# Optimization experiments

Measured on AMD Instinct MI355X. Metric: run time of the kernel, lower is better.

The kernel has to match this reference:

```python
import jax, jax.numpy as jnp
import numpy as np

H = 2048      # hidden_size
K = 16        # n_memory_tokens
NQ = K + 2    # extraction queries (+halt, +value)
NH = 4        # extraction heads
HD = H // NH  # head dim = 512
FFN = 2 * H   # ffn_mult=2
MAXE = 128    # memory buffer capacity (full -> eviction path)
B, S = 4, 4096
EPS = 1e-6


def setup_inputs() -> dict:
    key = jax.random.key(0)
    ks = jax.random.split(key, 20)
    r = lambda i, shape, s=0.02: jax.random.normal(ks[i], shape, jnp.float32) * s
    return {
        "hidden_states": jax.random.normal(ks[0], (B, S, H), jnp.float32),
        "buf_entries": jax.random.normal(ks[1], (MAXE, H), jnp.float32),
        "buf_priorities": jax.random.uniform(ks[2], (MAXE,), jnp.float32),
        "queries": r(3, (NQ, H)),
        "Wq": r(4, (H, H)), "Wk": r(5, (H, H)), "Wv": r(6, (H, H)), "Wo": r(7, (H, H)),
        "ln_w": jnp.ones((H,), jnp.float32),
        "Wgate": r(8, (FFN, H)), "Wup": r(9, (FFN, H)), "Wdown": r(10, (H, FFN)),
        "Wp": r(11, (1, H)), "bp": jnp.full((1,), 0.5, jnp.float32),
        "Wh": r(12, (1, H)), "bh": jnp.full((1,), 1.0, jnp.float32),
        "V1": r(13, (H, 2 * H)), "b1": jnp.zeros((H,), jnp.float32),
        "V2": r(14, (H // 4, H)), "b2": jnp.zeros((H // 4,), jnp.float32),
        "V3": jnp.zeros((1, H // 4), jnp.float32), "b3": jnp.zeros((1,), jnp.float32),
    }


def reference(hidden_states, buf_entries, buf_priorities, queries,
              Wq, Wk, Wv, Wo, ln_w, Wgate, Wup, Wdown,
              Wp, bp, Wh, bh, V1, b1, V2, b2, V3, b3):
    b = hidden_states.shape[0]
    # --- cross-attention: NQ learned queries attend over hidden states ---
    q = (queries @ Wq.T).reshape(NQ, NH, HD)               # queries shared across batch
    k = (hidden_states @ Wk.T).reshape(b, -1, NH, HD)      # (b, s, h, d)
    v = (hidden_states @ Wv.T).reshape(b, -1, NH, HD)
    scores = jnp.einsum('qhd,bshd->bhqs', q, k) / jnp.sqrt(jnp.float32(HD))
    attn = jax.nn.softmax(scores, axis=-1)
    out = jnp.einsum('bhqs,bshd->bqhd', attn, v).reshape(b, NQ, H)
    extracted = out @ Wo.T
    memory_raw = extracted[:, :K]            # (b, K, H)
    confidence_vec = extracted[:, K]         # (b, H)
    value_vec = extracted[:, K + 1]          # (b, H)
    # --- RMSNorm + SwiGLU FFN residual (dropout = identity in eval) ---
    ms = jnp.mean(memory_raw * memory_raw, axis=-1, keepdims=True)
    xn = memory_raw * jax.lax.rsqrt(ms + EPS) * ln_w
    ffn = (jax.nn.silu(xn @ Wgate.T) * (xn @ Wup.T)) @ Wdown.T
    memory = memory_raw + ffn
    # --- heads ---
    priority = jax.nn.sigmoid(memory @ Wp.T + bp)[..., 0]          # (b, K)
    confidence = jax.nn.sigmoid(confidence_vec @ Wh.T + bh)[..., 0]  # (b,)
    value_input = jnp.concatenate([value_vec, hidden_states[:, -1, :]], axis=-1)
    h1 = jax.nn.silu(value_input @ V1.T + b1)
    h2 = jax.nn.silu(h1 @ V2.T + b2)
    value = (h2 @ V3.T + b3)[..., 0]                               # (b,)
    # --- MemoryBuffer.store with full buffer: sequential priority eviction ---
    # (torch loops K times with argmin().item() host syncs; lax.scan preserves
    #  the sequential compare-and-replace semantics in one fused program)
    vecs = jax.lax.stop_gradient(memory[0])     # store detaches; uses batch 0
    pris = jax.lax.stop_gradient(priority[0])

    def step(carry, xp):
        ent, pr = carry
        vec, p = xp
        idx = jnp.argmin(pr)
        take = p > pr[idx]
        ent = ent.at[idx].set(jnp.where(take, vec, ent[idx]))
        pr = pr.at[idx].set(jnp.where(take, p, pr[idx]))
        return (ent, pr), None

    (new_entries, new_priorities), _ = jax.lax.scan(step, (buf_entries, buf_priorities), (vecs, pris))
    return memory, priority, confidence, value, new_entries, new_priorities
```

## Files before the change

kernel.cpp:

```cpp
#include <hip/hip_runtime.h>

#define SS    4096
#define HH    2048
#define NQQ   18
#define QH    72
#define SCALE_F 0.044194173824159216f

#define OUT_MEM     0
#define OUT_PRI     131072
#define OUT_CONF    131136
#define OUT_VAL     131140
#define OUT_ENT     131144
#define OUT_NEWPRI  393288

typedef float  f32x4  __attribute__((ext_vector_type(4)));
typedef __bf16 bf16x8 __attribute__((ext_vector_type(8)));

#define DEVFN static __device__ __forceinline__

DEVFN bf16x8 pack8(f32x4 lo, f32x4 hi){
  bf16x8 r;
  #pragma unroll
  for (int i = 0; i < 4; i++){ r[i] = (__bf16)lo[i]; r[i+4] = (__bf16)hi[i]; }
  return r;
}
DEVFN float siluf(float x){ return x / (1.f + expf(-x)); }
DEVFN float block_sum(float v, float* sb){
  #pragma unroll
  for (int o = 32; o > 0; o >>= 1) v += __shfl_xor(v, o);
  int wid = threadIdx.x >> 6, lane = threadIdx.x & 63;
  if (lane == 0) sb[wid] = v;
  __syncthreads();
  v = sb[0] + sb[1] + sb[2] + sb[3];
  __syncthreads();
  return v;
}

template<int MF, int KC, bool HSEL>
__global__ __launch_bounds__(256) void gemm_bt(
    const __bf16* __restrict__ A, int Kf,
    const float* __restrict__ B0, float* __restrict__ C0,
    const float* __restrict__ B1, float* __restrict__ C1,
    int N)
{
  constexpr int Mp = 16 * MF;
  const int lane = threadIdx.x & 63, w = threadIdx.x >> 6;
  const int n0 = blockIdx.x * 64 + w * 16;
  const int k0 = blockIdx.y * KC * 32;
  const float* B = blockIdx.z ? B1 : B0;
  float* Cp      = blockIdx.z ? C1 : C0;
  const __bf16* aBase = A + (HSEL ? (long)(n0 >> 9) * Mp * Kf : 0)
                          + (long)(lane & 15) * Kf + k0 + 8 * (lane >> 4);
  const float* bBase = B + (long)(n0 + (lane & 15)) * Kf + k0 + 8 * (lane >> 4);
  f32x4 acc[MF];
  #pragma unroll
  for (int m = 0; m < MF; m++) acc[m] = (f32x4)(0.f);
  #pragma unroll 4
  for (int c = 0; c < KC; c++){
    f32x4 lo = *reinterpret_cast<const f32x4*>(bBase + c * 32);
    f32x4 hi = *reinterpret_cast<const f32x4*>(bBase + c * 32 + 4);
    bf16x8 bb = pack8(lo, hi);
    #pragma unroll
    for (int m = 0; m < MF; m++){
      bf16x8 aa = *reinterpret_cast<const bf16x8*>(aBase + (long)m * 16 * Kf + c * 32);
      acc[m] = __builtin_amdgcn_mfma_f32_16x16x32_bf16(aa, bb, acc[m], 0, 0, 0);
    }
  }
  float* cp = Cp + (long)blockIdx.y * Mp * N;
  int row0 = 4 * (lane >> 4), col = n0 + (lane & 15);
  #pragma unroll
  for (int m = 0; m < MF; m++)
    #pragma unroll
    for (int r = 0; r < 4; r++)
      cp[(long)(m * 16 + row0 + r) * N + col] = acc[m][r];
}

template<int MF, int KC>
__global__ __launch_bounds__(256) void gemm_abnat(
    const __bf16* __restrict__ A, long aBatch, int aStride,
    const float* __restrict__ Bn, long bBatch,
    float* __restrict__ Cp, long cBatch,
    int N)
{
  constexpr int Mp = 16 * MF;
  const int lane = threadIdx.x & 63, w = threadIdx.x >> 6;
  const int z = blockIdx.z;
  const int n0 = blockIdx.x * 64 + w * 16;
  const int k0 = blockIdx.y * KC * 32;
  const __bf16* aBase = A + z * aBatch + (long)(lane & 15) * aStride + k0 + 8 * (lane >> 4);
  const float* bBase = Bn + z * bBatch + (long)(k0 + 8 * (lane >> 4)) * N + n0 + (lane & 15);
  f32x4 acc[MF];
  #pragma unroll
  for (int m = 0; m < MF; m++) acc[m] = (f32x4)(0.f);
  #pragma unroll 2
  for (int c = 0; c < KC; c++){
    const float* bp = bBase + (long)c * 32 * N;
    bf16x8 bb;
    #pragma unroll
    for (int j = 0; j < 8; j++) bb[j] = (__bf16)bp[(long)j * N];
    #pragma unroll
    for (int m = 0; m < MF; m++){
      bf16x8 aa = *reinterpret_cast<const bf16x8*>(aBase + (long)m * 16 * aStride + c * 32);
      acc[m] = __builtin_amdgcn_mfma_f32_16x16x32_bf16(aa, bb, acc[m], 0, 0, 0);
    }
  }
  float* cp = Cp + z * cBatch + (long)blockIdx.y * Mp * N;
  int row0 = 4 * (lane >> 4), col = n0 + (lane & 15);
  #pragma unroll
  for (int m = 0; m < MF; m++)
    #pragma unroll
    for (int r = 0; r < 4; r++)
      cp[(long)(m * 16 + row0 + r) * N + col] = acc[m][r];
}

template<int KC>
__global__ __launch_bounds__(256) void gemm_pass1(
    const float* __restrict__ hs, const __bf16* __restrict__ qk,
    float* __restrict__ Sp)
{
  const int lane = threadIdx.x & 63, w = threadIdx.x >> 6;
  const int b = blockIdx.z;
  const int s0 = blockIdx.x * 64 + w * 16;
  const int k0 = blockIdx.y * KC * 32;
  const float* aBase = hs + ((long)b * SS + s0 + (lane & 15)) * HH + k0 + 8 * (lane >> 4);
  const __bf16* bBase = qk + (long)(lane & 15) * HH + k0 + 8 * (lane >> 4);
  f32x4 acc[5];
  #pragma unroll
  for (int n = 0; n < 5; n++) acc[n] = (f32x4)(0.f);
  #pragma unroll 4
  for (int c = 0; c < KC; c++){
    f32x4 lo = *reinterpret_cast<const f32x4*>(aBase + c * 32);
    f32x4 hi = *reinterpret_cast<const f32x4*>(aBase + c * 32 + 4);
    bf16x8 aa = pack8(lo, hi);
    #pragma unroll
    for (int n = 0; n < 5; n++){
      bf16x8 bb = *reinterpret_cast<const bf16x8*>(bBase + (long)n * 16 * HH + c * 32);
      acc[n] = __builtin_amdgcn_mfma_f32_16x16x32_bf16(aa, bb, acc[n], 0, 0, 0);
    }
  }
  float* sp = Sp + ((long)blockIdx.y * 4 + b) * 80 * SS;
  int scol = s0 + 4 * (lane >> 4);
  #pragma unroll
  for (int n = 0; n < 5; n++){
    int qh = n * 16 + (lane & 15);
    *reinterpret_cast<f32x4*>(sp + (long)qh * SS + scol) = acc[n];
  }
}

__global__ void k_prep_qA(const float* __restrict__ queries, __bf16* __restrict__ qA){
  int i = blockIdx.x * 256 + threadIdx.x;
  int r = i >> 11;
  qA[i] = (__bf16)((r < NQQ) ? queries[i] : 0.f);
}
__global__ void k_mkQ2(const float* __restrict__ q_p, __bf16* __restrict__ Q2){
  int i = blockIdx.x * 256 + threadIdx.x;
  int qh = i >> 11, e = i & 2047;
  float v = 0.f;
  if (qh < QH){
    int h = qh / NQQ, qq = qh - h * NQQ;
    if ((e >> 9) == h){
      float s = 0.f;
      #pragma unroll
      for (int y = 0; y < 16; y++) s += q_p[(long)y * 32 * 2048 + qq * 2048 + e];
      v = s * SCALE_F;
    }
  }
  Q2[i] = (__bf16)v;
}
__global__ void k_mkqk(const float* __restrict__ qk_p, __bf16* __restrict__ qk_bf){
  int i = blockIdx.x * 256 + threadIdx.x;
  float s = 0.f;
  #pragma unroll
  for (int y = 0; y < 16; y++) s += qk_p[(long)y * 80 * 2048 + i];
  qk_bf[i] = (__bf16)s;
}
__global__ __launch_bounds__(256) void k_softmax(const float* __restrict__ Sp, __bf16* __restrict__ attn){
  int qh = blockIdx.x, b = blockIdx.y;
  __bf16* arow = attn + ((long)b * 80 + qh) * SS;
  if (qh >= QH){
    #pragma unroll
    for (int it = 0; it < 16; it++) arow[threadIdx.x + 256 * it] = (__bf16)0.f;
    return;
  }
  const float* r0 = Sp + ((long)b * 80 + qh) * SS;
  const long ys = (long)4 * 80 * SS;
  float x[16]; float mx = -1e30f;
  #pragma unroll
  for (int it = 0; it < 16; it++){
    int s = threadIdx.x + 256 * it;
    x[it] = (r0[s] + r0[s + ys]) + (r0[s + 2 * ys] + r0[s + 3 * ys]);
    mx = fmaxf(mx, x[it]);
  }
  __shared__ float sb[8];
  #pragma unroll
  for (int o = 32; o > 0; o >>= 1) mx = fmaxf(mx, __shfl_xor(mx, o));
  int wid = threadIdx.x >> 6, lane = threadIdx.x & 63;
  if (lane == 0) sb[wid] = mx;
  __syncthreads();
  mx = fmaxf(fmaxf(sb[0], sb[1]), fmaxf(sb[2], sb[3]));
  float sum = 0.f;
  #pragma unroll
  for (int it = 0; it < 16; it++){ x[it] = expf(x[it] - mx); sum += x[it]; }
  #pragma unroll
  for (int o = 32; o > 0; o >>= 1) sum += __shfl_xor(sum, o);
  if (lane == 0) sb[4 + wid] = sum;
  __syncthreads();
  sum = sb[4] + sb[5] + sb[6] + sb[7];
  float inv = 1.f / sum;
  #pragma unroll
  for (int it = 0; it < 16; it++) arow[threadIdx.x + 256 * it] = (__bf16)(x[it] * inv);
}
__global__ void k_pack_wv(const float* __restrict__ w_p, __bf16* __restrict__ Apack){
  int i = blockIdx.x * 256 + threadIdx.x;
  int h = i / (80 * 2048);
  int r = (i / 2048) % 80;
  int e = i & 2047;
  float v = 0.f;
  if (r < QH){
    int b = r / NQQ, qq = r - b * NQQ;
    const float* base = w_p + ((long)b * 8 * 80 + (h * NQQ + qq)) * 2048 + e;
    #pragma unroll
    for (int y = 0; y < 8; y++) v += base[(long)y * 80 * 2048];
  }
  Apack[i] = (__bf16)v;
}
__global__ void k_sum_outB(const float* __restrict__ outB_p, __bf16* __restrict__ outB){
  int i = blockIdx.x * 256 + threadIdx.x;
  float s = 0.f;
  #pragma unroll
  for (int y = 0; y < 16; y++) s += outB_p[(long)y * 80 * 2048 + i];
  outB[i] = (__bf16)s;
}
__global__ __launch_bounds__(256) void k_rms(const float* __restrict__ ext_p, const float* __restrict__ ln_w,
                                             const float* __restrict__ hs,
                                             float* __restrict__ extracted, __bf16* __restrict__ xnb,
                                             __bf16* __restrict__ vi){
  int r = blockIdx.x;
  if (r >= 80){
    if (r < 84){
      int b = r - 80;
      const float* src = hs + ((long)b * SS + (SS - 1)) * HH;
      #pragma unroll
      for (int it = 0; it < 8; it++){
        int e = threadIdx.x + 256 * it;
        vi[(long)b * 4096 + 2048 + e] = (__bf16)src[e];
      }
    } else {
      int row = 4 + (r - 84);
      #pragma unroll
      for (int it = 0; it < 16; it++)
        vi[(long)row * 4096 + threadIdx.x + 256 * it] = (__bf16)0.f;
    }
    return;
  }
  float xv[8]; float ss = 0.f;
  #pragma unroll
  for (int it = 0; it < 8; it++){
    int e = threadIdx.x + 256 * it;
    float s = 0.f;
    #pragma unroll
    for (int y = 0; y < 16; y++) s += ext_p[((long)y * 80 + r) * 2048 + e];
    extracted[(long)r * 2048 + e] = s;
    xv[it] = s;
    ss += s * s;
  }
  if (r >= QH) return;
  int b = r / NQQ, qq = r - b * NQQ;
  if (qq < 16){
    __shared__ float sb[4];
    ss = block_sum(ss, sb);
    float inv = 1.f / sqrtf(ss * (1.f / 2048.f) + 1e-6f);
    __bf16* dst = xnb + (long)(b * 16 + qq) * HH;
    #pragma unroll
    for (int it = 0; it < 8; it++){
      int e = threadIdx.x + 256 * it;
      dst[e] = (__bf16)(xv[it] * inv * ln_w[e]);
    }
  } else if (qq == 17){
    #pragma unroll
    for (int it = 0; it < 8; it++){
      int e = threadIdx.x + 256 * it;
      vi[(long)b * 4096 + e] = (__bf16)xv[it];
    }
  }
}
__global__ void k_act(const float* __restrict__ gate_p, const float* __restrict__ up_p,
                      __bf16* __restrict__ hb){
  int i = blockIdx.x * 256 + threadIdx.x;
  float g = 0.f, u = 0.f;
  #pragma unroll
  for (int y = 0; y < 4; y++){
    g += gate_p[(long)y * 64 * 4096 + i];
    u += up_p[(long)y * 64 * 4096 + i];
  }
  hb[i] = (__bf16)(siluf(g) * u);
}
__global__ void k_h1act(const float* __restrict__ h1_p, const float* __restrict__ b1,
                        __bf16* __restrict__ h1s){
  int i = blockIdx.x * 256 + threadIdx.x;
  int r = i >> 11, e = i & 2047;
  float v = 0.f;
  if (r < 4){
    float s = 0.f;
    #pragma unroll
    for (int y = 0; y < 16; y++) s += h1_p[(long)y * 16 * 2048 + i];
    v = siluf(s + b1[e]);
  }
  h1s[i] = (__bf16)v;
}
__global__ __launch_bounds__(256) void k_epilogue(
    const float* __restrict__ extracted, const float* __restrict__ ffn_p,
    const float* __restrict__ h2_p,
    const float* __restrict__ Wp, const float* __restrict__ bp,
    const float* __restrict__ Wh, const float* __restrict__ bh,
    const float* __restrict__ b2, const float* __restrict__ V3, const float* __restrict__ b3,
    float* __restrict__ out)
{
  __shared__ float sb[4];
  int blk = blockIdx.x;
  if (blk < 64){
    int b = blk >> 4, qq = blk & 15;
    const float* ext = extracted + (long)(b * NQQ + qq) * HH;
    float pv = 0.f;
    #pragma unroll
    for (int it = 0; it < 8; it++){
      int e = threadIdx.x + 256 * it;
      float f = 0.f;
      #pragma unroll
      for (int y = 0; y < 8; y++) f += ffn_p[((long)y * 64 + blk) * 2048 + e];
      float m = ext[e] + f;
      out[OUT_MEM + (long)blk * 2048 + e] = m;
      pv += m * Wp[e];
    }
    pv = block_sum(pv, sb);
    if (threadIdx.x == 0) out[OUT_PRI + blk] = 1.f / (1.f + expf(-(pv + bp[0])));
  } else if (blk < 68){
    int b = blk - 64;
    const float* m = extracted + (long)(b * NQQ + 16) * HH;
    float v = 0.f;
    #pragma unroll
    for (int it = 0; it < 8; it++){ int e = threadIdx.x + 256 * it; v += m[e] * Wh[e]; }
    v = block_sum(v, sb);
    if (threadIdx.x == 0) out[OUT_CONF + b] = 1.f / (1.f + expf(-(v + bh[0])));
  } else {
    int b = blk - 68;
    float v = 0.f;
    #pragma unroll
    for (int it = 0; it < 2; it++){
      int j = threadIdx.x + 256 * it;
      float s = 0.f;
      #pragma unroll
      for (int y = 0; y < 16; y++) s += h2_p[(long)y * 16 * 512 + b * 512 + j];
      v += siluf(s + b2[j]) * V3[j];
    }
    v = block_sum(v, sb);
    if (threadIdx.x == 0) out[OUT_VAL + b] = v + b3[0];
  }
}
__global__ void k_scan(const float* __restrict__ buf_pri, const float* __restrict__ out_ro,
                       float* __restrict__ out, int* __restrict__ tw){
  int lane = threadIdx.x;
  float pr0 = buf_pri[lane], pr1 = buf_pri[lane + 64];
  int tw0 = -1, tw1 = -1;
  for (int i = 0; i < 16; i++){
    float p = out_ro[OUT_PRI + i];
    float v; int idx;
    if (pr0 <= pr1){ v = pr0; idx = lane; } else { v = pr1; idx = lane + 64; }
    #pragma unroll
    for (int o = 32; o > 0; o >>= 1){
      float ov = __shfl_xor(v, o);
      int   oi = __shfl_xor(idx, o);
      if (ov < v || (ov == v && oi < idx)){ v = ov; idx = oi; }
    }
    if (p > v){
      if (idx == lane)          { pr0 = p; tw0 = i; }
      else if (idx == lane + 64){ pr1 = p; tw1 = i; }
    }
  }
  out[OUT_NEWPRI + lane]      = pr0;
  out[OUT_NEWPRI + lane + 64] = pr1;
  tw[lane] = tw0; tw[lane + 64] = tw1;
}
__global__ void k_entries(const float* __restrict__ buf_ent, const float* __restrict__ out_ro,
                          const int* __restrict__ tw, float* __restrict__ out){
  int row = blockIdx.x;
  int t = tw[row];
  const f32x4* s = reinterpret_cast<const f32x4*>(
      (t < 0) ? (buf_ent + (long)row * HH) : (out_ro + OUT_MEM + (long)t * HH));
  f32x4* d = reinterpret_cast<f32x4*>(out + OUT_ENT + (long)row * HH);
  #pragma unroll
  for (int i = 0; i < 2; i++) d[threadIdx.x + 256 * i] = s[threadIdx.x + 256 * i];
}

extern "C" void kernel_launch(void* const* d_in, const int* in_sizes, int n_in,
                              void* d_out, int out_size, void* d_ws, size_t ws_size,
                              hipStream_t stream)
{
  const float* hs      = (const float*)d_in[0];
  const float* buf_ent = (const float*)d_in[1];
  const float* buf_pri = (const float*)d_in[2];
  const float* queries = (const float*)d_in[3];
  const float* Wq  = (const float*)d_in[4];
  const float* Wk  = (const float*)d_in[5];
  const float* Wv  = (const float*)d_in[6];
  const float* Wo  = (const float*)d_in[7];
  const float* ln_w= (const float*)d_in[8];
  const float* Wgate=(const float*)d_in[9];
  const float* Wup = (const float*)d_in[10];
  const float* Wdown=(const float*)d_in[11];
  const float* Wp  = (const float*)d_in[12];
  const float* bp  = (const float*)d_in[13];
  const float* Wh  = (const float*)d_in[14];
  const float* bh  = (const float*)d_in[15];
  const float* V1  = (const float*)d_in[16];
  const float* b1  = (const float*)d_in[17];
  const float* V2  = (const float*)d_in[18];
  const float* b2  = (const float*)d_in[19];
  const float* V3  = (const float*)d_in[20];
  const float* b3  = (const float*)d_in[21];
  float* out = (float*)d_out;
  char* ws = (char*)d_ws;

  float* q_p      = (float*)(ws + 0);
  float* qk_p     = (float*)(ws + 0);
  float* scores_p = (float*)(ws + 0);
  float* w_p      = (float*)(ws + 0);
  float* outB_p   = (float*)(ws + 0);
  float* ext_p    = (float*)(ws + 0);
  float* gate_p   = (float*)(ws + 0);
  float* up_p     = (float*)(ws + 4194304);
  float* ffn_p    = (float*)(ws + 0);
  __bf16* qA    = (__bf16*)(ws + 20971520);
  __bf16* Q2    = (__bf16*)(ws + 21102592);
  __bf16* qk_bf = (__bf16*)(ws + 21430272);
  __bf16* attn  = (__bf16*)(ws + 21757952);
  __bf16* Apack = (__bf16*)(ws + 24379392);
  __bf16* outB  = (__bf16*)(ws + 25690112);
  float*  extracted = (float*)(ws + 26017792);
  __bf16* xnb   = (__bf16*)(ws + 26673152);
  __bf16* hb    = (__bf16*)(ws + 26935296);
  __bf16* vi    = (__bf16*)(ws + 27459584);
  __bf16* h1s   = (__bf16*)(ws + 27590656);
  float*  h1_p  = (float*)(ws + 27656192);
  float*  h2_p  = (float*)(ws + 29753344);
  int*    tw    = (int*)  (ws + 30277632);

  k_prep_qA<<<256, 256, 0, stream>>>(queries, qA);
  gemm_bt<2, 4, false><<<dim3(32, 16, 1), 256, 0, stream>>>(qA, 2048, Wq, q_p, Wq, q_p, 2048);
  k_mkQ2<<<640, 256, 0, stream>>>(q_p, Q2);
  gemm_abnat<5, 4><<<dim3(32, 16, 1), 256, 0, stream>>>(Q2, 0, 2048, Wk, 0, qk_p, 0, 2048);
  k_mkqk<<<640, 256, 0, stream>>>(qk_p, qk_bf);
  gemm_pass1<16><<<dim3(64, 4, 4), 256, 0, stream>>>(hs, qk_bf, scores_p);
  k_softmax<<<dim3(80, 4), 256, 0, stream>>>(scores_p, attn);
  gemm_abnat<5, 16><<<dim3(32, 8, 4), 256, 0, stream>>>(attn, 80L * 4096, 4096,
      hs, (long)SS * HH, w_p, 8L * 80 * 2048, 2048);
  k_pack_wv<<<2560, 256, 0, stream>>>(w_p, Apack);
  gemm_bt<5, 4, true><<<dim3(32, 16, 1), 256, 0, stream>>>(Apack, 2048, Wv, outB_p, Wv, outB_p, 2048);
  k_sum_outB<<<640, 256, 0, stream>>>(outB_p, outB);
  gemm_bt<5, 4, false><<<dim3(32, 16, 1), 256, 0, stream>>>(outB, 2048, Wo, ext_p, Wo, ext_p, 2048);
  k_rms<<<96, 256, 0, stream>>>(ext_p, ln_w, hs, extracted, xnb, vi);
  gemm_bt<4, 16, false><<<dim3(64, 4, 2), 256, 0, stream>>>(xnb, 2048, Wgate, gate_p, Wup, up_p, 4096);
  gemm_bt<1, 8, false><<<dim3(32, 16, 1), 256, 0, stream>>>(vi, 4096, V1, h1_p, V1, h1_p, 2048);
  k_act<<<1024, 256, 0, stream>>>(gate_p, up_p, hb);
  k_h1act<<<128, 256, 0, stream>>>(h1_p, b1, h1s);
  gemm_bt<4, 16, false><<<dim3(32, 8, 1), 256, 0, stream>>>(hb, 4096, Wdown, ffn_p, Wdown, ffn_p, 2048);
  gemm_bt<1, 4, false><<<dim3(8, 16, 1), 256, 0, stream>>>(h1s, 2048, V2, h2_p, V2, h2_p, 512);
  k_epilogue<<<72, 256, 0, stream>>>(extracted, ffn_p, h2_p, Wp, bp, Wh, bh, b2, V3, b3, out);
  k_scan<<<1, 64, 0, stream>>>(buf_pri, out, out, tw);
  k_entries<<<128, 256, 0, stream>>>(buf_ent, out, tw, out);
}
```

Before: 282.2 us.

## Fuse small pre- and post-attention stages into two cooperative persistent kernels

```diff
diff --git a/kernel.cpp b/kernel.cpp
--- a/kernel.cpp
+++ b/kernel.cpp
@@ -1,4 +1,6 @@
 #include <hip/hip_runtime.h>
+#include <hip/hip_cooperative_groups.h>
+namespace cg = cooperative_groups;
 
 #define SS    4096
 #define HH    2048
@@ -37,7 +39,7 @@
 }
 
 template<int MF, int KC, bool HSEL>
-__global__ __launch_bounds__(256) void gemm_bt(
+DEVFN void gemm_bt_body(int bx, int by, bool zsel,
     const __bf16* __restrict__ A, int Kf,
     const float* __restrict__ B0, float* __restrict__ C0,
     const float* __restrict__ B1, float* __restrict__ C1,
@@ -45,10 +47,10 @@
 {
   constexpr int Mp = 16 * MF;
   const int lane = threadIdx.x & 63, w = threadIdx.x >> 6;
-  const int n0 = blockIdx.x * 64 + w * 16;
-  const int k0 = blockIdx.y * KC * 32;
-  const float* B = blockIdx.z ? B1 : B0;
-  float* Cp      = blockIdx.z ? C1 : C0;
+  const int n0 = bx * 64 + w * 16;
+  const int k0 = by * KC * 32;
+  const float* B = zsel ? B1 : B0;
+  float* Cp      = zsel ? C1 : C0;
   const __bf16* aBase = A + (HSEL ? (long)(n0 >> 9) * Mp * Kf : 0)
                           + (long)(lane & 15) * Kf + k0 + 8 * (lane >> 4);
   const float* bBase = B + (long)(n0 + (lane & 15)) * Kf + k0 + 8 * (lane >> 4);
@@ -66,7 +68,7 @@
       acc[m] = __builtin_amdgcn_mfma_f32_16x16x32_bf16(aa, bb, acc[m], 0, 0, 0);
     }
   }
-  float* cp = Cp + (long)blockIdx.y * Mp * N;
+  float* cp = Cp + (long)by * Mp * N;
   int row0 = 4 * (lane >> 4), col = n0 + (lane & 15);
   #pragma unroll
   for (int m = 0; m < MF; m++)
@@ -76,7 +78,7 @@
 }
 
 template<int MF, int KC>
-__global__ __launch_bounds__(256) void gemm_abnat(
+DEVFN void gemm_abnat_body(int bx, int by, int bz,
     const __bf16* __restrict__ A, long aBatch, int aStride,
     const float* __restrict__ Bn, long bBatch,
     float* __restrict__ Cp, long cBatch,
@@ -84,11 +86,10 @@
 {
   constexpr int Mp = 16 * MF;
   const int lane = threadIdx.x & 63, w = threadIdx.x >> 6;
-  const int z = blockIdx.z;
-  const int n0 = blockIdx.x * 64 + w * 16;
-  const int k0 = blockIdx.y * KC * 32;
-  const __bf16* aBase = A + z * aBatch + (long)(lane & 15) * aStride + k0 + 8 * (lane >> 4);
-  const float* bBase = Bn + z * bBatch + (long)(k0 + 8 * (lane >> 4)) * N + n0 + (lane & 15);
+  const int n0 = bx * 64 + w * 16;
+  const int k0 = by * KC * 32;
+  const __bf16* aBase = A + bz * aBatch + (long)(lane & 15) * aStride + k0 + 8 * (lane >> 4);
+  const float* bBase = Bn + bz * bBatch + (long)(k0 + 8 * (lane >> 4)) * N + n0 + (lane & 15);
   f32x4 acc[MF];
   #pragma unroll
   for (int m = 0; m < MF; m++) acc[m] = (f32x4)(0.f);
@@ -104,7 +105,7 @@
       acc[m] = __builtin_amdgcn_mfma_f32_16x16x32_bf16(aa, bb, acc[m], 0, 0, 0);
     }
   }
-  float* cp = Cp + z * cBatch + (long)blockIdx.y * Mp * N;
+  float* cp = Cp + bz * cBatch + (long)by * Mp * N;
   int row0 = 4 * (lane >> 4), col = n0 + (lane & 15);
   #pragma unroll
   for (int m = 0; m < MF; m++)
@@ -146,33 +147,13 @@
     *reinterpret_cast<f32x4*>(sp + (long)qh * SS + scol) = acc[n];
   }
 }
-
-__global__ void k_prep_qA(const float* __restrict__ queries, __bf16* __restrict__ qA){
-  int i = blockIdx.x * 256 + threadIdx.x;
-  int r = i >> 11;
-  qA[i] = (__bf16)((r < NQQ) ? queries[i] : 0.f);
-}
-__global__ void k_mkQ2(const float* __restrict__ q_p, __bf16* __restrict__ Q2){
-  int i = blockIdx.x * 256 + threadIdx.x;
-  int qh = i >> 11, e = i & 2047;
-  float v = 0.f;
-  if (qh < QH){
-    int h = qh / NQQ, qq = qh - h * NQQ;
-    if ((e >> 9) == h){
-      float s = 0.f;
-      #pragma unroll
-      for (int y = 0; y < 16; y++) s += q_p[(long)y * 32 * 2048 + qq * 2048 + e];
-      v = s * SCALE_F;
-    }
-  }
-  Q2[i] = (__bf16)v;
-}
-__global__ void k_mkqk(const float* __restrict__ qk_p, __bf16* __restrict__ qk_bf){
-  int i = blockIdx.x * 256 + threadIdx.x;
-  float s = 0.f;
-  #pragma unroll
-  for (int y = 0; y < 16; y++) s += qk_p[(long)y * 80 * 2048 + i];
-  qk_bf[i] = (__bf16)s;
+template<int MF, int KC>
+__global__ __launch_bounds__(256) void gemm_abnat(
+    const __bf16* __restrict__ A, long aBatch, int aStride,
+    const float* __restrict__ Bn, long bBatch,
+    float* __restrict__ Cp, long cBatch, int N)
+{
+  gemm_abnat_body<MF, KC>(blockIdx.x, blockIdx.y, blockIdx.z, A, aBatch, aStride, Bn, bBatch, Cp, cBatch, N);
 }
 __global__ __launch_bounds__(256) void k_softmax(const float* __restrict__ Sp, __bf16* __restrict__ attn){
   int qh = blockIdx.x, b = blockIdx.y;
@@ -210,186 +191,251 @@
   #pragma unroll
   for (int it = 0; it < 16; it++) arow[threadIdx.x + 256 * it] = (__bf16)(x[it] * inv);
 }
-__global__ void k_pack_wv(const float* __restrict__ w_p, __bf16* __restrict__ Apack){
-  int i = blockIdx.x * 256 + threadIdx.x;
-  int h = i / (80 * 2048);
-  int r = (i / 2048) % 80;
-  int e = i & 2047;
-  float v = 0.f;
-  if (r < QH){
-    int b = r / NQQ, qq = r - b * NQQ;
-    const float* base = w_p + ((long)b * 8 * 80 + (h * NQQ + qq)) * 2048 + e;
-    #pragma unroll
-    for (int y = 0; y < 8; y++) v += base[(long)y * 80 * 2048];
-  }
-  Apack[i] = (__bf16)v;
-}
-__global__ void k_sum_outB(const float* __restrict__ outB_p, __bf16* __restrict__ outB){
-  int i = blockIdx.x * 256 + threadIdx.x;
-  float s = 0.f;
-  #pragma unroll
-  for (int y = 0; y < 16; y++) s += outB_p[(long)y * 80 * 2048 + i];
-  outB[i] = (__bf16)s;
-}
-__global__ __launch_bounds__(256) void k_rms(const float* __restrict__ ext_p, const float* __restrict__ ln_w,
-                                             const float* __restrict__ hs,
-                                             float* __restrict__ extracted, __bf16* __restrict__ xnb,
-                                             __bf16* __restrict__ vi){
-  int r = blockIdx.x;
-  if (r >= 80){
-    if (r < 84){
-      int b = r - 80;
-      const float* src = hs + ((long)b * SS + (SS - 1)) * HH;
+
+struct PA {
+  const float* queries; const float* Wq; const float* Wk;
+  __bf16* qA; float* q_p; __bf16* Q2; float* qk_p; __bf16* qk_bf;
+};
+__global__ __launch_bounds__(256, 2) void k_coopA(PA p){
+  cg::grid_group g = cg::this_grid();
+  const int bid = blockIdx.x, tid = threadIdx.x;
+  { int i = bid * 256 + tid;
+    if (i < 32 * 2048){ int r = i >> 11; p.qA[i] = (__bf16)((r < NQQ) ? p.queries[i] : 0.f); } }
+  g.sync();
+  gemm_bt_body<2, 4, false>(bid & 31, bid >> 5, false, p.qA, 2048, p.Wq, p.q_p, p.Wq, p.q_p, 2048);
+  g.sync();
+  for (int j = tid; j < 320; j += 256){
+    int i = bid * 320 + j;
+    int qh = i >> 11, e = i & 2047;
+    float v = 0.f;
+    if (qh < QH){
+      int h = qh / NQQ, qq = qh - h * NQQ;
+      if ((e >> 9) == h){
+        float s = 0.f;
+        #pragma unroll
+        for (int y = 0; y < 16; y++) s += p.q_p[(long)y * 32 * 2048 + qq * 2048 + e];
+        v = s * SCALE_F;
+      }
+    }
+    p.Q2[i] = (__bf16)v;
+  }
+  g.sync();
+  gemm_abnat_body<5, 4>(bid & 31, bid >> 5, 0, p.Q2, 0, 2048, p.Wk, 0, p.qk_p, 0, 2048);
+  g.sync();
+  for (int j = tid; j < 320; j += 256){
+    int i = bid * 320 + j;
+    float s = 0.f;
+    #pragma unroll
+    for (int y = 0; y < 16; y++) s += p.qk_p[(long)y * 80 * 2048 + i];
+    p.qk_bf[i] = (__bf16)s;
+  }
+}
+
+struct PB {
+  const float* hs; const float* buf_ent; const float* buf_pri;
+  const float* Wv; const float* Wo; const float* ln_w;
+  const float* Wgate; const float* Wup; const float* Wdown;
+  const float* Wp; const float* bp; const float* Wh; const float* bh;
+  const float* V1; const float* b1; const float* V2; const float* b2;
+  const float* V3; const float* b3;
+  const float* w_p; __bf16* Apack; float* outB_p; __bf16* outB;
+  float* ext_p; float* extracted; __bf16* xnb; __bf16* vi;
+  float* gate_p; float* up_p; __bf16* hb; float* h1_p; __bf16* h1s;
+  float* ffn_p; float* h2_p; float* out;
+};
+__global__ __launch_bounds__(256, 2) void k_coopB(PB p){
+  cg::grid_group g = cg::this_grid();
+  const int bid = blockIdx.x, tid = threadIdx.x;
+  __shared__ float sb[8];
+  __shared__ int tws;
+  for (int j = tid; j < 1280; j += 256){
+    long i = (long)bid * 1280 + j;
+    int h = (int)(i / (80 * 2048));
+    int r = (int)((i / 2048) % 80);
+    int e = (int)(i & 2047);
+    float v = 0.f;
+    if (r < QH){
+      int b = r / NQQ, qq = r - b * NQQ;
+      const float* base = p.w_p + ((long)b * 8 * 80 + (h * NQQ + qq)) * 2048 + e;
+      #pragma unroll
+      for (int y = 0; y < 8; y++) v += base[(long)y * 80 * 2048];
+    }
+    p.Apack[i] = (__bf16)v;
+  }
+  g.sync();
+  gemm_bt_body<5, 4, true>(bid & 31, bid >> 5, false, p.Apack, 2048, p.Wv, p.outB_p, p.Wv, p.outB_p, 2048);
+  g.sync();
+  for (int j = tid; j < 320; j += 256){
+    int i = bid * 320 + j;
+    float s = 0.f;
+    #pragma unroll
+    for (int y = 0; y < 16; y++) s += p.outB_p[(long)y * 80 * 2048 + i];
+    p.outB[i] = (__bf16)s;
+  }
+  g.sync();
+  gemm_bt_body<5, 4, false>(bid & 31, bid >> 5, false, p.outB, 2048, p.Wo, p.ext_p, p.Wo, p.ext_p, 2048);
+  g.sync();
+  { int r = bid;
+    if (r >= 80 && r < 96){
+      if (r < 84){
+        int b = r - 80;
+        const float* src = p.hs + ((long)b * SS + (SS - 1)) * HH;
+        #pragma unroll
+        for (int it = 0; it < 8; it++){
+          int e = tid + 256 * it;
+          p.vi[(long)b * 4096 + 2048 + e] = (__bf16)src[e];
+        }
+      } else {
+        int row = 4 + (r - 84);
+        #pragma unroll
+        for (int it = 0; it < 16; it++)
+          p.vi[(long)row * 4096 + tid + 256 * it] = (__bf16)0.f;
+      }
+    } else if (r < 80){
+      float xv[8]; float ss = 0.f;
       #pragma unroll
       for (int it = 0; it < 8; it++){
-        int e = threadIdx.x + 256 * it;
-        vi[(long)b * 4096 + 2048 + e] = (__bf16)src[e];
-      }
-    } else {
-      int row = 4 + (r - 84);
-      #pragma unroll
-      for (int it = 0; it < 16; it++)
-        vi[(long)row * 4096 + threadIdx.x + 256 * it] = (__bf16)0.f;
-    }
-    return;
-  }
-  float xv[8]; float ss = 0.f;
-  #pragma unroll
-  for (int it = 0; it < 8; it++){
-    int e = threadIdx.x + 256 * it;
-    float s = 0.f;
-    #pragma unroll
-    for (int y = 0; y < 16; y++) s += ext_p[((long)y * 80 + r) * 2048 + e];
-    extracted[(long)r * 2048 + e] = s;
-    xv[it] = s;
-    ss += s * s;
-  }
-  if (r >= QH) return;
-  int b = r / NQQ, qq = r - b * NQQ;
-  if (qq < 16){
-    __shared__ float sb[4];
-    ss = block_sum(ss, sb);
-    float inv = 1.f / sqrtf(ss * (1.f / 2048.f) + 1e-6f);
-    __bf16* dst = xnb + (long)(b * 16 + qq) * HH;
-    #pragma unroll
-    for (int it = 0; it < 8; it++){
-      int e = threadIdx.x + 256 * it;
-      dst[e] = (__bf16)(xv[it] * inv * ln_w[e]);
-    }
-  } else if (qq == 17){
-    #pragma unroll
-    for (int it = 0; it < 8; it++){
-      int e = threadIdx.x + 256 * it;
-      vi[(long)b * 4096 + e] = (__bf16)xv[it];
-    }
-  }
-}
-__global__ void k_act(const float* __restrict__ gate_p, const float* __restrict__ up_p,
-                      __bf16* __restrict__ hb){
-  int i = blockIdx.x * 256 + threadIdx.x;
-  float g = 0.f, u = 0.f;
-  #pragma unroll
-  for (int y = 0; y < 4; y++){
-    g += gate_p[(long)y * 64 * 4096 + i];
-    u += up_p[(long)y * 64 * 4096 + i];
-  }
-  hb[i] = (__bf16)(siluf(g) * u);
-}
-__global__ void k_h1act(const float* __restrict__ h1_p, const float* __restrict__ b1,
-                        __bf16* __restrict__ h1s){
-  int i = blockIdx.x * 256 + threadIdx.x;
-  int r = i >> 11, e = i & 2047;
-  float v = 0.f;
-  if (r < 4){
-    float s = 0.f;
-    #pragma unroll
-    for (int y = 0; y < 16; y++) s += h1_p[(long)y * 16 * 2048 + i];
-    v = siluf(s + b1[e]);
-  }
-  h1s[i] = (__bf16)v;
-}
-__global__ __launch_bounds__(256) void k_epilogue(
-    const float* __restrict__ extracted, const float* __restrict__ ffn_p,
-    const float* __restrict__ h2_p,
-    const float* __restrict__ Wp, const float* __restrict__ bp,
-    const float* __restrict__ Wh, const float* __restrict__ bh,
-    const float* __restrict__ b2, const float* __restrict__ V3, const float* __restrict__ b3,
-    float* __restrict__ out)
-{
-  __shared__ float sb[4];
-  int blk = blockIdx.x;
-  if (blk < 64){
-    int b = blk >> 4, qq = blk & 15;
-    const float* ext = extracted + (long)(b * NQQ + qq) * HH;
-    float pv = 0.f;
-    #pragma unroll
-    for (int it = 0; it < 8; it++){
-      int e = threadIdx.x + 256 * it;
-      float f = 0.f;
-      #pragma unroll
-      for (int y = 0; y < 8; y++) f += ffn_p[((long)y * 64 + blk) * 2048 + e];
-      float m = ext[e] + f;
-      out[OUT_MEM + (long)blk * 2048 + e] = m;
-      pv += m * Wp[e];
-    }
-    pv = block_sum(pv, sb);
-    if (threadIdx.x == 0) out[OUT_PRI + blk] = 1.f / (1.f + expf(-(pv + bp[0])));
-  } else if (blk < 68){
-    int b = blk - 64;
-    const float* m = extracted + (long)(b * NQQ + 16) * HH;
+        int e = tid + 256 * it;
+        float s = 0.f;
+        #pragma unroll
+        for (int y = 0; y < 16; y++) s += p.ext_p[((long)y * 80 + r) * 2048 + e];
+        p.extracted[(long)r * 2048 + e] = s;
+        xv[it] = s;
+        ss += s * s;
+      }
+      if (r < QH){
+        int b = r / NQQ, qq = r - b * NQQ;
+        if (qq < 16){
+          ss = block_sum(ss, sb);
+          float inv = 1.f / sqrtf(ss * (1.f / 2048.f) + 1e-6f);
+          __bf16* dst = p.xnb + (long)(b * 16 + qq) * HH;
+          #pragma unroll
+          for (int it = 0; it < 8; it++){
+            int e = tid + 256 * it;
+            dst[e] = (__bf16)(xv[it] * inv * p.ln_w[e]);
+          }
+        } else if (qq == 17){
+          #pragma unroll
+          for (int it = 0; it < 8; it++){
+            int e = tid + 256 * it;
+            p.vi[(long)b * 4096 + e] = (__bf16)xv[it];
+          }
+        }
+      }
+    }
+  }
+  g.sync();
+  if (bid < 256){
+    int t = bid;
+    gemm_bt_body<4, 32, false>(t & 63, (t >> 6) & 1, (t >> 7) != 0,
+                               p.xnb, 2048, p.Wgate, p.gate_p, p.Wup, p.up_p, 4096);
+  } else {
+    int t = bid - 256;
+    gemm_bt_body<1, 16, false>(t & 31, t >> 5, false, p.vi, 4096, p.V1, p.h1_p, p.V1, p.h1_p, 2048);
+  }
+  g.sync();
+  for (int j = tid; j < 512; j += 256){
+    long i = (long)bid * 512 + j;
+    float gv = p.gate_p[i] + p.gate_p[(long)64 * 4096 + i];
+    float uv = p.up_p[i]   + p.up_p[(long)64 * 4096 + i];
+    p.hb[i] = (__bf16)(siluf(gv) * uv);
+  }
+  if (bid < 128){
+    int i = bid * 256 + tid;
+    int r = i >> 11, e = i & 2047;
     float v = 0.f;
-    #pragma unroll
-    for (int it = 0; it < 8; it++){ int e = threadIdx.x + 256 * it; v += m[e] * Wh[e]; }
-    v = block_sum(v, sb);
-    if (threadIdx.x == 0) out[OUT_CONF + b] = 1.f / (1.f + expf(-(v + bh[0])));
-  } else {
-    int b = blk - 68;
-    float v = 0.f;
-    #pragma unroll
-    for (int it = 0; it < 2; it++){
-      int j = threadIdx.x + 256 * it;
+    if (r < 4){
       float s = 0.f;
       #pragma unroll
-      for (int y = 0; y < 16; y++) s += h2_p[(long)y * 16 * 512 + b * 512 + j];
-      v += siluf(s + b2[j]) * V3[j];
-    }
-    v = block_sum(v, sb);
-    if (threadIdx.x == 0) out[OUT_VAL + b] = v + b3[0];
-  }
-}
-__global__ void k_scan(const float* __restrict__ buf_pri, const float* __restrict__ out_ro,
-                       float* __restrict__ out, int* __restrict__ tw){
-  int lane = threadIdx.x;
-  float pr0 = buf_pri[lane], pr1 = buf_pri[lane + 64];
-  int tw0 = -1, tw1 = -1;
-  for (int i = 0; i < 16; i++){
-    float p = out_ro[OUT_PRI + i];
-    float v; int idx;
-    if (pr0 <= pr1){ v = pr0; idx = lane; } else { v = pr1; idx = lane + 64; }
-    #pragma unroll
-    for (int o = 32; o > 0; o >>= 1){
-      float ov = __shfl_xor(v, o);
-      int   oi = __shfl_xor(idx, o);
-      if (ov < v || (ov == v && oi < idx)){ v = ov; idx = oi; }
-    }
-    if (p > v){
-      if (idx == lane)          { pr0 = p; tw0 = i; }
-      else if (idx == lane + 64){ pr1 = p; tw1 = i; }
-    }
-  }
-  out[OUT_NEWPRI + lane]      = pr0;
-  out[OUT_NEWPRI + lane + 64] = pr1;
-  tw[lane] = tw0; tw[lane + 64] = tw1;
-}
-__global__ void k_entries(const float* __restrict__ buf_ent, const float* __restrict__ out_ro,
-                          const int* __restrict__ tw, float* __restrict__ out){
-  int row = blockIdx.x;
-  int t = tw[row];
-  const f32x4* s = reinterpret_cast<const f32x4*>(
-      (t < 0) ? (buf_ent + (long)row * HH) : (out_ro + OUT_MEM + (long)t * HH));
-  f32x4* d = reinterpret_cast<f32x4*>(out + OUT_ENT + (long)row * HH);
-  #pragma unroll
-  for (int i = 0; i < 2; i++) d[threadIdx.x + 256 * i] = s[threadIdx.x + 256 * i];
+      for (int y = 0; y < 8; y++) s += p.h1_p[(long)y * 16 * 2048 + i];
+      v = siluf(s + p.b1[e]);
+    }
+    p.h1s[i] = (__bf16)v;
+  }
+  g.sync();
+  if (bid < 256){
+    int t = bid;
+    gemm_bt_body<4, 16, false>(t & 31, t >> 5, false, p.hb, 4096, p.Wdown, p.ffn_p, p.Wdown, p.ffn_p, 2048);
+  } else if (bid < 384){
+    int t = bid - 256;
+    gemm_bt_body<1, 4, false>(t & 7, t >> 3, false, p.h1s, 2048, p.V2, p.h2_p, p.V2, p.h2_p, 512);
+  }
+  g.sync();
+  { int blk = bid;
+    if (blk < 64){
+      int b = blk >> 4, qq = blk & 15;
+      const float* ext = p.extracted + (long)(b * NQQ + qq) * HH;
+      float pv = 0.f;
+      #pragma unroll
+      for (int it = 0; it < 8; it++){
+        int e = tid + 256 * it;
+        float f = 0.f;
+        #pragma unroll
+        for (int y = 0; y < 8; y++) f += p.ffn_p[((long)y * 64 + blk) * 2048 + e];
+        float m = ext[e] + f;
+        p.out[OUT_MEM + (long)blk * 2048 + e] = m;
+        pv += m * p.Wp[e];
+      }
+      pv = block_sum(pv, sb);
+      if (tid == 0) p.out[OUT_PRI + blk] = 1.f / (1.f + expf(-(pv + p.bp[0])));
+    } else if (blk < 68){
+      int b = blk - 64;
+      const float* m = p.extracted + (long)(b * NQQ + 16) * HH;
+      float v = 0.f;
+      #pragma unroll
+      for (int it = 0; it < 8; it++){ int e = tid + 256 * it; v += m[e] * p.Wh[e]; }
+      v = block_sum(v, sb);
+      if (tid == 0) p.out[OUT_CONF + b] = 1.f / (1.f + expf(-(v + p.bh[0])));
+    } else if (blk < 72){
+      int b = blk - 68;
+      float v = 0.f;
+      #pragma unroll
+      for (int it = 0; it < 2; it++){
+        int j = tid + 256 * it;
+        float s = 0.f;
+        #pragma unroll
+        for (int y = 0; y < 16; y++) s += p.h2_p[(long)y * 16 * 512 + b * 512 + j];
+        v += siluf(s + p.b2[j]) * p.V3[j];
+      }
+      v = block_sum(v, sb);
+      if (tid == 0) p.out[OUT_VAL + b] = v + p.b3[0];
+    }
+  }
+  g.sync();
+  if (bid < 128){
+    if (tid < 64){
+      int lane = tid;
+      float pr0 = p.buf_pri[lane], pr1 = p.buf_pri[lane + 64];
+      int tw0 = -1, tw1 = -1;
+      for (int i = 0; i < 16; i++){
+        float pp = p.out[OUT_PRI + i];
+        float v; int idx;
+        if (pr0 <= pr1){ v = pr0; idx = lane; } else { v = pr1; idx = lane + 64; }
+        #pragma unroll
+        for (int o = 32; o > 0; o >>= 1){
+          float ov = __shfl_xor(v, o);
+          int   oi = __shfl_xor(idx, o);
+          if (ov < v || (ov == v && oi < idx)){ v = ov; idx = oi; }
+        }
+        if (pp > v){
+          if (idx == lane)          { pr0 = pp; tw0 = i; }
+          else if (idx == lane + 64){ pr1 = pp; tw1 = i; }
+        }
+      }
+      if (bid == 0){
+        p.out[OUT_NEWPRI + lane]      = pr0;
+        p.out[OUT_NEWPRI + lane + 64] = pr1;
+      }
+      if (lane == (bid & 63)) tws = (bid < 64) ? tw0 : tw1;
+    }
+    __syncthreads();
+    int t = tws;
+    const f32x4* s = reinterpret_cast<const f32x4*>(
+        (t < 0) ? (p.buf_ent + (long)bid * HH) : (p.out + OUT_MEM + (long)t * HH));
+    f32x4* d = reinterpret_cast<f32x4*>(p.out + OUT_ENT + (long)bid * HH);
+    #pragma unroll
+    for (int i = 0; i < 2; i++) d[tid + 256 * i] = s[tid + 256 * i];
+  }
 }
 
 extern "C" void kernel_launch(void* const* d_in, const int* in_sizes, int n_in,
@@ -428,7 +474,7 @@
   float* outB_p   = (float*)(ws + 0);
   float* ext_p    = (float*)(ws + 0);
   float* gate_p   = (float*)(ws + 0);
-  float* up_p     = (float*)(ws + 4194304);
+  float* up_p     = (float*)(ws + 2097152);
   float* ffn_p    = (float*)(ws + 0);
   __bf16* qA    = (__bf16*)(ws + 20971520);
   __bf16* Q2    = (__bf16*)(ws + 21102592);
@@ -443,29 +489,20 @@
   __bf16* h1s   = (__bf16*)(ws + 27590656);
   float*  h1_p  = (float*)(ws + 27656192);
   float*  h2_p  = (float*)(ws + 29753344);
-  int*    tw    = (int*)  (ws + 30277632);
-
-  k_prep_qA<<<256, 256, 0, stream>>>(queries, qA);
-  gemm_bt<2, 4, false><<<dim3(32, 16, 1), 256, 0, stream>>>(qA, 2048, Wq, q_p, Wq, q_p, 2048);
-  k_mkQ2<<<640, 256, 0, stream>>>(q_p, Q2);
-  gemm_abnat<5, 4><<<dim3(32, 16, 1), 256, 0, stream>>>(Q2, 0, 2048, Wk, 0, qk_p, 0, 2048);
-  k_mkqk<<<640, 256, 0, stream>>>(qk_p, qk_bf);
+
+  PA pa{queries, Wq, Wk, qA, q_p, Q2, qk_p, qk_bf};
+  void* argsA[] = {&pa};
+  hipLaunchCooperativeKernel(reinterpret_cast<void*>(k_coopA),
+                             dim3(512), dim3(256), argsA, 0, stream);
   gemm_pass1<16><<<dim3(64, 4, 4), 256, 0, stream>>>(hs, qk_bf, scores_p);
   k_softmax<<<dim3(80, 4), 256, 0, stream>>>(scores_p, attn);
   gemm_abnat<5, 16><<<dim3(32, 8, 4), 256, 0, stream>>>(attn, 80L * 4096, 4096,
       hs, (long)SS * HH, w_p, 8L * 80 * 2048, 2048);
-  k_pack_wv<<<2560, 256, 0, stream>>>(w_p, Apack);
-  gemm_bt<5, 4, true><<<dim3(32, 16, 1), 256, 0, stream>>>(Apack, 2048, Wv, outB_p, Wv, outB_p, 2048);
-  k_sum_outB<<<640, 256, 0, stream>>>(outB_p, outB);
-  gemm_bt<5, 4, false><<<dim3(32, 16, 1), 256, 0, stream>>>(outB, 2048, Wo, ext_p, Wo, ext_p, 2048);
-  k_rms<<<96, 256, 0, stream>>>(ext_p, ln_w, hs, extracted, xnb, vi);
-  gemm_bt<4, 16, false><<<dim3(64, 4, 2), 256, 0, stream>>>(xnb, 2048, Wgate, gate_p, Wup, up_p, 4096);
-  gemm_bt<1, 8, false><<<dim3(32, 16, 1), 256, 0, stream>>>(vi, 4096, V1, h1_p, V1, h1_p, 2048);
-  k_act<<<1024, 256, 0, stream>>>(gate_p, up_p, hb);
-  k_h1act<<<128, 256, 0, stream>>>(h1_p, b1, h1s);
-  gemm_bt<4, 16, false><<<dim3(32, 8, 1), 256, 0, stream>>>(hb, 4096, Wdown, ffn_p, Wdown, ffn_p, 2048);
-  gemm_bt<1, 4, false><<<dim3(8, 16, 1), 256, 0, stream>>>(h1s, 2048, V2, h2_p, V2, h2_p, 512);
-  k_epilogue<<<72, 256, 0, stream>>>(extracted, ffn_p, h2_p, Wp, bp, Wh, bh, b2, V3, b3, out);
-  k_scan<<<1, 64, 0, stream>>>(buf_pri, out, out, tw);
-  k_entries<<<128, 256, 0, stream>>>(buf_ent, out, tw, out);
-}
+  PB pb{hs, buf_ent, buf_pri, Wv, Wo, ln_w, Wgate, Wup, Wdown,
+        Wp, bp, Wh, bh, V1, b1, V2, b2, V3, b3,
+        w_p, Apack, outB_p, outB, ext_p, extracted, xnb, vi,
+        gate_p, up_p, hb, h1_p, h1s, ffn_p, h2_p, out};
+  void* argsB[] = {&pb};
+  hipLaunchCooperativeKernel(reinterpret_cast<void*>(k_coopB),
+                             dim3(512), dim3(256), argsB, 0, stream);
+}
```

Result: slower. 1.009 ms (+257.4%).
